# Optimization experiments

Measured on AMD Instinct MI355X. Metric: run time of the kernel, lower is better.

Reference implementation:

```python
import jax, jax.numpy as jnp
import numpy as np

# Static ragged block structure: (num_graphs_in_bucket, n) -> block tensor (B, n, n, C)
BLOCKS = [(128, 32), (64, 48), (32, 64), (16, 96)]
C = 64
DEPTH = 2
EPS = 1e-5
N_TOTAL = sum(b * n * n for b, n in BLOCKS)  # 557056


def _mlp(h, w, b):
    # stack of DEPTH Linear(C->C) + ReLU layers (1x1 convs in the torch module)
    for d in range(w.shape[0]):
        h = jax.nn.relu(jnp.einsum('...i,oi->...o', h, w[d]) + b[d])
    return h


def _bn(h, g, b, m, v):
    # eval-mode BatchNorm1d with running stats
    return g * (h - m) * jax.lax.rsqrt(v + EPS) + b


def setup_inputs() -> dict:
    key = jax.random.key(0)
    ks = jax.random.split(key, 8)
    s = 1.0 / np.sqrt(C)

    def lin(k):
        return jax.random.normal(k, (C, C), jnp.float32) * s

    return dict(
        x=jax.random.normal(ks[0], (N_TOTAL, C), jnp.float32),
        w_m1=jax.random.normal(ks[1], (DEPTH, C, C), jnp.float32) * s,
        b_m1=jnp.zeros((DEPTH, C), jnp.float32),
        w_m2=jax.random.normal(ks[2], (DEPTH, C, C), jnp.float32) * s,
        b_m2=jnp.zeros((DEPTH, C), jnp.float32),
        W_skip=lin(ks[3]), b_skip=jnp.zeros((C,), jnp.float32),
        W_u1=lin(ks[4]), b_u1=jnp.zeros((C,), jnp.float32),
        g1=jnp.ones((C,), jnp.float32), beta1=jnp.zeros((C,), jnp.float32),
        rm1=jnp.zeros((C,), jnp.float32), rv1=jnp.ones((C,), jnp.float32),
        W_u2=lin(ks[5]), b_u2=jnp.zeros((C,), jnp.float32),
        g2=jnp.ones((C,), jnp.float32), beta2=jnp.zeros((C,), jnp.float32),
        rm2=jnp.zeros((C,), jnp.float32), rv2=jnp.ones((C,), jnp.float32),
    )


def reference(x, w_m1, b_m1, w_m2, b_m2, W_skip, b_skip,
              W_u1, b_u1, g1, beta1, rm1, rv1,
              W_u2, b_u2, g2, beta2, rm2, rv2):
    # --- ragged split -> per-block PPGN-style matmul conv -> cat ---
    hs = []
    off = 0
    for (bnum, n) in BLOCKS:
        ln = bnum * n * n
        blk = x[off:off + ln].reshape(bnum, n, n, C)  # (B, n, n, C)
        m1 = _mlp(blk, w_m1, b_m1)
        m2 = _mlp(blk, w_m2, b_m2)
        # per-channel spatial matmul over the n x n block
        h = jnp.einsum('bijc,bjkc->bikc', m1, m2)
        hs.append(h.reshape(ln, C))
        off += ln
    hs2 = jnp.concatenate(hs, 0) + (x @ W_skip.T + b_skip)
    # --- update MLP: Linear-BN-ReLU-(Dropout eval=id)-Linear-BN-ReLU + residual ---
    u = jax.nn.relu(_bn(hs2 @ W_u1.T + b_u1, g1, beta1, rm1, rv1))
    u = jax.nn.relu(_bn(u @ W_u2.T + b_u2, g2, beta2, rm2, rv2))
    return u + hs2
```

## Files before the change

### kernel.cpp

```cpp
#include <hip/hip_runtime.h>
#include <hip/hip_bf16.h>

#define NT 557056
typedef __hip_bfloat16 bf16;
typedef __attribute__((ext_vector_type(8))) short short8;
typedef __attribute__((ext_vector_type(4))) short short4v;
typedef __attribute__((ext_vector_type(4))) float f32x4;


__device__ __forceinline__ short f2bs(float f){ bf16 h = __float2bfloat16(f); return *(short*)&h; }
__device__ __forceinline__ float s2f(short s){ bf16 h = *(bf16*)&s; return __bfloat162float(h); }

__device__ __forceinline__ short8 cvt8(float4 a, float4 b){
  short8 r;
  r[0]=f2bs(a.x); r[1]=f2bs(a.y); r[2]=f2bs(a.z); r[3]=f2bs(a.w);
  r[4]=f2bs(b.x); r[5]=f2bs(b.y); r[6]=f2bs(b.z); r[7]=f2bs(b.w);
  return r;
}
__device__ __forceinline__ short8 ldfrag(const float* __restrict__ p){
  return cvt8(*(const float4*)p, *(const float4*)(p + 4));
}
__device__ __forceinline__ short8 ldfrag_s(const float* __restrict__ p, float s){
  float4 a = *(const float4*)p, b = *(const float4*)(p + 4);
  a.x*=s; a.y*=s; a.z*=s; a.w*=s; b.x*=s; b.y*=s; b.z*=s; b.w*=s;
  return cvt8(a, b);
}
#define MFMA(a,b,c) __builtin_amdgcn_mfma_f32_16x16x32_bf16(a, b, c, 0, 0, 0)

#define LS 72

__global__ __launch_bounds__(256, 2) void k1_mlp(
    const float* __restrict__ x,
    const float* __restrict__ w_m1, const float* __restrict__ b_m1,
    const float* __restrict__ w_m2, const float* __restrict__ b_m2,
    bf16* __restrict__ m1t, bf16* __restrict__ m2t)
{
  __shared__ short yL[4][32][LS];
  const int tid = threadIdx.x;
  const int wv = tid >> 6, lane = tid & 63, r = lane & 15, g = lane >> 4;
  const int wid = blockIdx.x * 4 + wv;

  short8 wf[4][4][2];
  #pragma unroll
  for (int cb = 0; cb < 4; ++cb)
    #pragma unroll
    for (int s = 0; s < 2; ++s) {
      const int o = (cb*16 + r)*64 + s*32 + g*8;
      wf[0][cb][s] = ldfrag(w_m1 + o);
      wf[1][cb][s] = ldfrag(w_m1 + 4096 + o);
      wf[2][cb][s] = ldfrag(w_m2 + o);
      wf[3][cb][s] = ldfrag(w_m2 + 4096 + o);
    }
  f32x4 b0v[2][4];
  float b1v[2][4];
  #pragma unroll
  for (int m = 0; m < 2; ++m) {
    const float* bb = m ? b_m2 : b_m1;
    #pragma unroll
    for (int cb = 0; cb < 4; ++cb) {
      b0v[m][cb] = *(const f32x4*)(bb + cb*16 + 4*g);
      b1v[m][cb] = bb[64 + cb*16 + r];
    }
  }

  size_t pb = (size_t)wid * 128;

  float4 xr[8];
  #pragma unroll
  for (int h = 0; h < 2; ++h) {
    const float* xp = x + (pb + h*16 + r)*64 + g*8;
    xr[4*h+0] = *(const float4*)(xp);
    xr[4*h+1] = *(const float4*)(xp + 4);
    xr[4*h+2] = *(const float4*)(xp + 32);
    xr[4*h+3] = *(const float4*)(xp + 36);
  }

  for (int t = 0; t < 4; ++t, pb += 32) {
    short8 xf[2][2];
    xf[0][0] = cvt8(xr[0], xr[1]);  xf[0][1] = cvt8(xr[2], xr[3]);
    xf[1][0] = cvt8(xr[4], xr[5]);  xf[1][1] = cvt8(xr[6], xr[7]);
    if (t < 3) {
      #pragma unroll
      for (int h = 0; h < 2; ++h) {
        const float* xp = x + (pb + 32 + h*16 + r)*64 + g*8;
        xr[4*h+0] = *(const float4*)(xp);
        xr[4*h+1] = *(const float4*)(xp + 4);
        xr[4*h+2] = *(const float4*)(xp + 32);
        xr[4*h+3] = *(const float4*)(xp + 36);
      }
    }
    const size_t tbase = (pb >> 5) * 2048;
    #pragma unroll
    for (int m = 0; m < 2; ++m) {
      f32x4 acc[4][2];
      #pragma unroll
      for (int cb = 0; cb < 4; ++cb) { acc[cb][0] = b0v[m][cb]; acc[cb][1] = b0v[m][cb]; }
      #pragma unroll
      for (int cb = 0; cb < 4; ++cb)
        #pragma unroll
        for (int s = 0; s < 2; ++s) {
          acc[cb][0] = MFMA(wf[2*m][cb][s], xf[0][s], acc[cb][0]);
          acc[cb][1] = MFMA(wf[2*m][cb][s], xf[1][s], acc[cb][1]);
        }
      #pragma unroll
      for (int cb = 0; cb < 4; ++cb)
        #pragma unroll
        for (int th = 0; th < 2; ++th) {
          short4v v;
          #pragma unroll
          for (int q = 0; q < 4; ++q) v[q] = f2bs(fmaxf(acc[cb][th][q], 0.f));
          *(short4v*)&yL[wv][th*16 + r][cb*16 + 4*g] = v;
        }
      short8 af[2][2];
      #pragma unroll
      for (int th = 0; th < 2; ++th)
        #pragma unroll
        for (int s = 0; s < 2; ++s)
          af[th][s] = *(const short8*)&yL[wv][th*16 + r][s*32 + g*8];
      f32x4 acc2[4][2];
      #pragma unroll
      for (int cb = 0; cb < 4; ++cb) {
        const float bv = b1v[m][cb];
        acc2[cb][0] = (f32x4){bv,bv,bv,bv};
        acc2[cb][1] = (f32x4){bv,bv,bv,bv};
      }
      #pragma unroll
      for (int cb = 0; cb < 4; ++cb)
        #pragma unroll
        for (int s = 0; s < 2; ++s) {
          acc2[cb][0] = MFMA(af[0][s], wf[2*m+1][cb][s], acc2[cb][0]);
          acc2[cb][1] = MFMA(af[1][s], wf[2*m+1][cb][s], acc2[cb][1]);
        }
      bf16* op = m ? m2t : m1t;
      #pragma unroll
      for (int cb = 0; cb < 4; ++cb) {
        short8 v;
        #pragma unroll
        for (int th = 0; th < 2; ++th)
          #pragma unroll
          for (int q = 0; q < 4; ++q) v[th*4+q] = f2bs(fmaxf(acc2[cb][th][q], 0.f));
        *(short8*)(op + tbase + (cb*16 + r)*32 + g*8) = v;
      }
    }
  }
}

template<int N>
__global__ __launch_bounds__(256) void k2_spatial(
    const bf16* __restrict__ m1t, const bf16* __restrict__ m2t,
    bf16* __restrict__ ht, int off)
{
  constexpr int T = N / 16;
  constexpr int SA = N + 4;
  __shared__ __align__(16) float AT[N*SA];
  __shared__ __align__(16) float Bs[N*SA];
  const int b = blockIdx.x >> 6;
  const int c = blockIdx.x & 63;
  const size_t base_tile = ((size_t)off + (size_t)b * N * N) >> 5;
  const int tid = threadIdx.x;

  for (int idx8 = tid*8; idx8 < N*N; idx8 += 2048) {
    const size_t gaddr = (base_tile + (idx8 >> 5)) * 2048 + c*32 + (idx8 & 31);
    short8 a8 = *(const short8*)(m1t + gaddr);
    short8 b8 = *(const short8*)(m2t + gaddr);
    const int gsub = (idx8 & 31) >> 3;
    const int i0 = idx8 & ~31;
    #pragma unroll
    for (int th = 0; th < 2; ++th) {
      const int i = i0 + th*16 + 4*gsub;
      const int j = i / N, k0 = i - j*N;
      f32x4 bq;
      #pragma unroll
      for (int q = 0; q < 4; ++q) bq[q] = s2f(b8[th*4+q]);
      *(f32x4*)&Bs[j*SA + k0] = bq;
      #pragma unroll
      for (int q = 0; q < 4; ++q) AT[(k0+q)*SA + j] = s2f(a8[th*4+q]);
    }
  }
  __syncthreads();

  const int ti = tid >> 4, tk = tid & 15;
  float acc[T][T];
  #pragma unroll
  for (int ii = 0; ii < T; ++ii)
    #pragma unroll
    for (int kk = 0; kk < T; ++kk) acc[ii][kk] = 0.f;

  for (int j = 0; j < N; ++j) {
    const float* ar = &AT[j*SA + ti*T];
    const float* br = &Bs[j*SA + tk*T];
    float av[T], bv[T];
    if constexpr (T == 2) {
      float2 a2 = *(const float2*)ar; av[0]=a2.x; av[1]=a2.y;
      float2 b2 = *(const float2*)br; bv[0]=b2.x; bv[1]=b2.y;
    } else if constexpr (T == 3) {
      av[0]=ar[0]; av[1]=ar[1]; av[2]=ar[2];
      bv[0]=br[0]; bv[1]=br[1]; bv[2]=br[2];
    } else if constexpr (T == 4) {
      float4 a4 = *(const float4*)ar; av[0]=a4.x; av[1]=a4.y; av[2]=a4.z; av[3]=a4.w;
      float4 b4 = *(const float4*)br; bv[0]=b4.x; bv[1]=b4.y; bv[2]=b4.z; bv[3]=b4.w;
    } else {
      #pragma unroll
      for (int p = 0; p < 3; ++p) {
        float2 a2 = *(const float2*)(ar + 2*p); av[2*p]=a2.x; av[2*p+1]=a2.y;
        float2 b2 = *(const float2*)(br + 2*p); bv[2*p]=b2.x; bv[2*p+1]=b2.y;
      }
    }
    #pragma unroll
    for (int ii = 0; ii < T; ++ii)
      #pragma unroll
      for (int kk = 0; kk < T; ++kk)
        acc[ii][kk] = fmaf(av[ii], bv[kk], acc[ii][kk]);
  }

  __syncthreads();
  float* Cf = AT;
  #pragma unroll
  for (int ii = 0; ii < T; ++ii)
    #pragma unroll
    for (int kk = 0; kk < T; ++kk)
      Cf[(ti*T + ii)*N + tk*T + kk] = acc[ii][kk];
  __syncthreads();

  for (int idx8 = tid*8; idx8 < N*N; idx8 += 2048) {
    const int i0 = idx8 & ~31, gsub = (idx8 & 31) >> 3;
    f32x4 lo = *(const f32x4*)&Cf[i0 + 4*gsub];
    f32x4 hi = *(const f32x4*)&Cf[i0 + 16 + 4*gsub];
    short8 v;
    #pragma unroll
    for (int q = 0; q < 4; ++q) { v[q] = f2bs(lo[q]); v[4+q] = f2bs(hi[q]); }
    const size_t gaddr = (base_tile + (idx8 >> 5)) * 2048 + c*32 + (idx8 & 31);
    *(short8*)(ht + gaddr) = v;
  }
}

__global__ __launch_bounds__(256, 2) void k3_update(
    const float* __restrict__ x, const bf16* __restrict__ ht,
    const float* __restrict__ Wskip, const float* __restrict__ bskip,
    const float* __restrict__ Wu1, const float* __restrict__ bu1,
    const float* __restrict__ g1, const float* __restrict__ be1,
    const float* __restrict__ rm1, const float* __restrict__ rv1,
    const float* __restrict__ Wu2, const float* __restrict__ bu2,
    const float* __restrict__ g2, const float* __restrict__ be2,
    const float* __restrict__ rm2, const float* __restrict__ rv2,
    float* __restrict__ out)
{
  __shared__ short hs2L[4][32][LS];
  __shared__ short u1L[4][32][LS];
  const int tid = threadIdx.x;
  const int wv = tid >> 6, lane = tid & 63, r = lane & 15, g = lane >> 4;
  const int wid = blockIdx.x * 4 + wv;

  short8 wsk[4][2], w1f[4][2], w2f[4][2];
  float bskv[4];
  f32x4 b1c[4], b2c[4];
  #pragma unroll
  for (int cb = 0; cb < 4; ++cb) {
    const int row = cb*16 + r;
    const float s1 = g1[row] * rsqrtf(rv1[row] + 1e-5f);
    const float s2 = g2[row] * rsqrtf(rv2[row] + 1e-5f);
    #pragma unroll
    for (int s = 0; s < 2; ++s) {
      const int o = row*64 + s*32 + g*8;
      wsk[cb][s] = ldfrag(Wskip + o);
      w1f[cb][s] = ldfrag_s(Wu1 + o, s1);
      w2f[cb][s] = ldfrag_s(Wu2 + o, s2);
    }
    bskv[cb] = bskip[row];
    const int o4 = cb*16 + 4*g;
    f32x4 gg1 = *(const f32x4*)(g1 + o4),  vv1 = *(const f32x4*)(rv1 + o4);
    f32x4 mm1 = *(const f32x4*)(rm1 + o4), bb1 = *(const f32x4*)(be1 + o4);
    f32x4 u1b = *(const f32x4*)(bu1 + o4);
    f32x4 gg2 = *(const f32x4*)(g2 + o4),  vv2 = *(const f32x4*)(rv2 + o4);
    f32x4 mm2 = *(const f32x4*)(rm2 + o4), bb2 = *(const f32x4*)(be2 + o4);
    f32x4 u2b = *(const f32x4*)(bu2 + o4);
    #pragma unroll
    for (int q = 0; q < 4; ++q) {
      const float c1 = gg1[q] * rsqrtf(vv1[q] + 1e-5f);
      b1c[cb][q] = bb1[q] + (u1b[q] - mm1[q]) * c1;
      const float c2 = gg2[q] * rsqrtf(vv2[q] + 1e-5f);
      b2c[cb][q] = bb2[q] + (u2b[q] - mm2[q]) * c2;
    }
  }

  size_t pb = (size_t)wid * 128;

  float4 xr[8];
  #pragma unroll
  for (int h = 0; h < 2; ++h) {
    const float* xp = x + (pb + h*16 + r)*64 + g*8;
    xr[4*h+0] = *(const float4*)(xp);
    xr[4*h+1] = *(const float4*)(xp + 4);
    xr[4*h+2] = *(const float4*)(xp + 32);
    xr[4*h+3] = *(const float4*)(xp + 36);
  }

  for (int t = 0; t < 4; ++t, pb += 32) {
    short8 xf[2][2];
    xf[0][0] = cvt8(xr[0], xr[1]);  xf[0][1] = cvt8(xr[2], xr[3]);
    xf[1][0] = cvt8(xr[4], xr[5]);  xf[1][1] = cvt8(xr[6], xr[7]);
    if (t < 3) {
      #pragma unroll
      for (int h = 0; h < 2; ++h) {
        const float* xp = x + (pb + 32 + h*16 + r)*64 + g*8;
        xr[4*h+0] = *(const float4*)(xp);
        xr[4*h+1] = *(const float4*)(xp + 4);
        xr[4*h+2] = *(const float4*)(xp + 32);
        xr[4*h+3] = *(const float4*)(xp + 36);
      }
    }
    const size_t tbase = (pb >> 5) * 2048;
    short8 hv8[4];
    #pragma unroll
    for (int cb = 0; cb < 4; ++cb)
      hv8[cb] = *(const short8*)(ht + tbase + (cb*16 + r)*32 + g*8);

    f32x4 acc[4][2];
    #pragma unroll
    for (int cb = 0; cb < 4; ++cb) {
      acc[cb][0] = (f32x4){bskv[cb], bskv[cb], bskv[cb], bskv[cb]};
      acc[cb][1] = acc[cb][0];
    }
    #pragma unroll
    for (int cb = 0; cb < 4; ++cb)
      #pragma unroll
      for (int s = 0; s < 2; ++s) {
        acc[cb][0] = MFMA(xf[0][s], wsk[cb][s], acc[cb][0]);
        acc[cb][1] = MFMA(xf[1][s], wsk[cb][s], acc[cb][1]);
      }
    #pragma unroll
    for (int cb = 0; cb < 4; ++cb)
      #pragma unroll
      for (int th = 0; th < 2; ++th)
        #pragma unroll
        for (int q = 0; q < 4; ++q) acc[cb][th][q] += s2f(hv8[cb][th*4+q]);
    #pragma unroll
    for (int cb = 0; cb < 4; ++cb)
      #pragma unroll
      for (int th = 0; th < 2; ++th)
        #pragma unroll
        for (int q = 0; q < 4; ++q)
          hs2L[wv][th*16 + 4*g + q][cb*16 + r] = f2bs(acc[cb][th][q]);
    short8 hf[2][2];
    #pragma unroll
    for (int th = 0; th < 2; ++th)
      #pragma unroll
      for (int s = 0; s < 2; ++s)
        hf[th][s] = *(const short8*)&hs2L[wv][th*16 + r][s*32 + g*8];

    f32x4 a1[4][2];
    #pragma unroll
    for (int cb = 0; cb < 4; ++cb) { a1[cb][0] = b1c[cb]; a1[cb][1] = b1c[cb]; }
    #pragma unroll
    for (int cb = 0; cb < 4; ++cb)
      #pragma unroll
      for (int s = 0; s < 2; ++s) {
        a1[cb][0] = MFMA(w1f[cb][s], hf[0][s], a1[cb][0]);
        a1[cb][1] = MFMA(w1f[cb][s], hf[1][s], a1[cb][1]);
      }
    #pragma unroll
    for (int cb = 0; cb < 4; ++cb)
      #pragma unroll
      for (int th = 0; th < 2; ++th) {
        short4v v;
        #pragma unroll
        for (int q = 0; q < 4; ++q) v[q] = f2bs(fmaxf(a1[cb][th][q], 0.f));
        *(short4v*)&u1L[wv][th*16 + r][cb*16 + 4*g] = v;
      }
    short8 uf[2][2];
    #pragma unroll
    for (int th = 0; th < 2; ++th)
      #pragma unroll
      for (int s = 0; s < 2; ++s)
        uf[th][s] = *(const short8*)&u1L[wv][th*16 + r][s*32 + g*8];

    f32x4 a2[4][2];
    #pragma unroll
    for (int cb = 0; cb < 4; ++cb) { a2[cb][0] = b2c[cb]; a2[cb][1] = b2c[cb]; }
    #pragma unroll
    for (int cb = 0; cb < 4; ++cb)
      #pragma unroll
      for (int s = 0; s < 2; ++s) {
        a2[cb][0] = MFMA(w2f[cb][s], uf[0][s], a2[cb][0]);
        a2[cb][1] = MFMA(w2f[cb][s], uf[1][s], a2[cb][1]);
      }
    #pragma unroll
    for (int cb = 0; cb < 4; ++cb)
      #pragma unroll
      for (int th = 0; th < 2; ++th) {
        short4v hres = *(const short4v*)&hs2L[wv][th*16 + r][cb*16 + 4*g];
        f32x4 res;
        #pragma unroll
        for (int q = 0; q < 4; ++q)
          res[q] = fmaxf(a2[cb][th][q], 0.f) + s2f(hres[q]);
        *(f32x4*)(out + (pb + th*16 + r)*64 + cb*16 + 4*g) = res;
      }
  }
}

extern "C" void kernel_launch(void* const* d_in, const int* in_sizes, int n_in,
                              void* d_out, int out_size, void* d_ws, size_t ws_size,
                              hipStream_t stream) {
  const float* x     = (const float*)d_in[0];
  const float* w_m1  = (const float*)d_in[1];
  const float* b_m1  = (const float*)d_in[2];
  const float* w_m2  = (const float*)d_in[3];
  const float* b_m2  = (const float*)d_in[4];
  const float* Wskip = (const float*)d_in[5];
  const float* bskip = (const float*)d_in[6];
  const float* Wu1   = (const float*)d_in[7];
  const float* bu1   = (const float*)d_in[8];
  const float* g1    = (const float*)d_in[9];
  const float* be1   = (const float*)d_in[10];
  const float* rm1   = (const float*)d_in[11];
  const float* rv1   = (const float*)d_in[12];
  const float* Wu2   = (const float*)d_in[13];
  const float* bu2   = (const float*)d_in[14];
  const float* g2    = (const float*)d_in[15];
  const float* be2   = (const float*)d_in[16];
  const float* rm2   = (const float*)d_in[17];
  const float* rv2   = (const float*)d_in[18];
  float* out = (float*)d_out;

  bf16* m1t = (bf16*)d_ws;
  bf16* m2t = m1t + (size_t)64 * NT;
  bf16* ht  = m1t;

  k1_mlp<<<1088, 256, 0, stream>>>(x, w_m1, b_m1, w_m2, b_m2, m1t, m2t);

  k2_spatial<32><<<128*64, 256, 0, stream>>>(m1t, m2t, ht, 0);
  k2_spatial<48><<< 64*64, 256, 0, stream>>>(m1t, m2t, ht, 131072);
  k2_spatial<64><<< 32*64, 256, 0, stream>>>(m1t, m2t, ht, 278528);
  k2_spatial<96><<< 16*64, 256, 0, stream>>>(m1t, m2t, ht, 409600);

  k3_update<<<1088, 256, 0, stream>>>(x, ht, Wskip, bskip,
                                      Wu1, bu1, g1, be1, rm1, rv1,
                                      Wu2, bu2, g2, be2, rm2, rv2, out);
}
```

Baseline: 568.6 us.

## Replace scalar FP32 spatial matmul with bf16 MFMA kernel batching channels per block

The per-channel n×n spatial matmul kernel drops the FP32 FMA register-tiled loop and uses bf16 MFMA instructions reading fragments from LDS. Each block now processes several channels (CH), so global loads cover larger contiguous segments of the channel-interleaved layout. B is stored transposed and padded in LDS, and n=48 is zero-padded to the 32-wide K step. The added LDS staging and transposed scatter stores can cause bank conflicts, and inputs to the MFMA are in bf16 rather than being upcast to FP32.

New measurement: 544.6 us. 4.2% less time.

```diff
diff --git a/kernel.cpp b/kernel.cpp
--- a/kernel.cpp
+++ b/kernel.cpp
@@ -145,92 +145,92 @@
   }
 }
 
-template<int N>
-__global__ __launch_bounds__(256) void k2_spatial(
+template<int N, int CH, int NP, int CP>
+__global__ __launch_bounds__(256) void k2_mfma(
     const bf16* __restrict__ m1t, const bf16* __restrict__ m2t,
     bf16* __restrict__ ht, int off)
 {
-  constexpr int T = N / 16;
-  constexpr int SA = N + 4;
-  __shared__ __align__(16) float AT[N*SA];
-  __shared__ __align__(16) float Bs[N*SA];
-  const int b = blockIdx.x >> 6;
-  const int c = blockIdx.x & 63;
+  constexpr int TPB = N*N/32;
+  constexpr int NT16 = N/16;
+  constexpr int TPC = NT16*NT16;
+  constexpr int KS = (N + 31)/32;
+  constexpr int GRP = 64/CH;
+
+  __shared__ short Am[CH][N][NP];
+  __shared__ short Bt[CH][N][NP];
+  __shared__ short Cs[CH][N][CP];
+
+  const int tid = threadIdx.x;
+  const int grp = blockIdx.x % GRP;
+  const int b   = blockIdx.x / GRP;
+  const int c0  = grp * CH;
   const size_t base_tile = ((size_t)off + (size_t)b * N * N) >> 5;
-  const int tid = threadIdx.x;
-
-  for (int idx8 = tid*8; idx8 < N*N; idx8 += 2048) {
-    const size_t gaddr = (base_tile + (idx8 >> 5)) * 2048 + c*32 + (idx8 & 31);
-    short8 a8 = *(const short8*)(m1t + gaddr);
-    short8 b8 = *(const short8*)(m2t + gaddr);
-    const int gsub = (idx8 & 31) >> 3;
-    const int i0 = idx8 & ~31;
-    #pragma unroll
-    for (int th = 0; th < 2; ++th) {
-      const int i = i0 + th*16 + 4*gsub;
-      const int j = i / N, k0 = i - j*N;
-      f32x4 bq;
-      #pragma unroll
-      for (int q = 0; q < 4; ++q) bq[q] = s2f(b8[th*4+q]);
-      *(f32x4*)&Bs[j*SA + k0] = bq;
-      #pragma unroll
-      for (int q = 0; q < 4; ++q) AT[(k0+q)*SA + j] = s2f(a8[th*4+q]);
+
+  constexpr int UPT = CH * TPB * 4;
+  for (int u = tid; u < 2*UPT; u += 256) {
+    int uu = u;
+    const bf16* src = m1t;
+    bool isA = true;
+    if (uu >= UPT) { uu -= UPT; src = m2t; isA = false; }
+    const int a   = uu & 3;
+    const int cc  = (uu >> 2) % CH;
+    const int tau = (uu >> 2) / CH;
+    short8 v = *(const short8*)(src + (base_tile + tau)*2048 + (size_t)(c0+cc)*32 + a*8);
+    const int p0 = tau*32 + 4*a;
+    #pragma unroll
+    for (int h = 0; h < 2; ++h) {
+      const int p = p0 + h*16;
+      const int row = p / N, col = p % N;
+      if (isA) {
+        short4v w; w[0]=v[h*4+0]; w[1]=v[h*4+1]; w[2]=v[h*4+2]; w[3]=v[h*4+3];
+        *(short4v*)&Am[cc][row][col] = w;
+      } else {
+        #pragma unroll
+        for (int q = 0; q < 4; ++q) Bt[cc][col+q][row] = v[h*4+q];
+      }
+    }
+  }
+  if constexpr (N == 48) {
+    for (int u = tid; u < CH*N*4*2; u += 256) {
+      int uu = u; bool isA = uu < CH*N*4; if (!isA) uu -= CH*N*4;
+      const int seg = uu & 3, row = (uu>>2) % N, cc = (uu>>2) / N;
+      short4v z = {0,0,0,0};
+      if (isA) *(short4v*)&Am[cc][row][48 + seg*4] = z;
+      else     *(short4v*)&Bt[cc][row][48 + seg*4] = z;
     }
   }
   __syncthreads();
 
-  const int ti = tid >> 4, tk = tid & 15;
-  float acc[T][T];
-  #pragma unroll
-  for (int ii = 0; ii < T; ++ii)
-    #pragma unroll
-    for (int kk = 0; kk < T; ++kk) acc[ii][kk] = 0.f;
-
-  for (int j = 0; j < N; ++j) {
-    const float* ar = &AT[j*SA + ti*T];
-    const float* br = &Bs[j*SA + tk*T];
-    float av[T], bv[T];
-    if constexpr (T == 2) {
-      float2 a2 = *(const float2*)ar; av[0]=a2.x; av[1]=a2.y;
-      float2 b2 = *(const float2*)br; bv[0]=b2.x; bv[1]=b2.y;
-    } else if constexpr (T == 3) {
-      av[0]=ar[0]; av[1]=ar[1]; av[2]=ar[2];
-      bv[0]=br[0]; bv[1]=br[1]; bv[2]=br[2];
-    } else if constexpr (T == 4) {
-      float4 a4 = *(const float4*)ar; av[0]=a4.x; av[1]=a4.y; av[2]=a4.z; av[3]=a4.w;
-      float4 b4 = *(const float4*)br; bv[0]=b4.x; bv[1]=b4.y; bv[2]=b4.z; bv[3]=b4.w;
-    } else {
-      #pragma unroll
-      for (int p = 0; p < 3; ++p) {
-        float2 a2 = *(const float2*)(ar + 2*p); av[2*p]=a2.x; av[2*p+1]=a2.y;
-        float2 b2 = *(const float2*)(br + 2*p); bv[2*p]=b2.x; bv[2*p+1]=b2.y;
-      }
-    }
-    #pragma unroll
-    for (int ii = 0; ii < T; ++ii)
-      #pragma unroll
-      for (int kk = 0; kk < T; ++kk)
-        acc[ii][kk] = fmaf(av[ii], bv[kk], acc[ii][kk]);
-  }
-
+  const int wv = tid >> 6, lane = tid & 63, r = lane & 15, g = lane >> 4;
+  for (int idx = wv; idx < CH*TPC; idx += 4) {
+    const int cc = idx / TPC, t = idx % TPC;
+    const int i0 = (t / NT16) * 16, k0 = (t % NT16) * 16;
+    f32x4 acc = {0.f, 0.f, 0.f, 0.f};
+    #pragma unroll
+    for (int ks = 0; ks < KS; ++ks) {
+      short8 afr = *(const short8*)&Am[cc][i0 + r][ks*32 + g*8];
+      short8 bfr = *(const short8*)&Bt[cc][k0 + r][ks*32 + g*8];
+      acc = MFMA(afr, bfr, acc);
+    }
+    #pragma unroll
+    for (int q = 0; q < 4; ++q) Cs[cc][i0 + 4*g + q][k0 + r] = f2bs(acc[q]);
+  }
   __syncthreads();
-  float* Cf = AT;
-  #pragma unroll
-  for (int ii = 0; ii < T; ++ii)
-    #pragma unroll
-    for (int kk = 0; kk < T; ++kk)
-      Cf[(ti*T + ii)*N + tk*T + kk] = acc[ii][kk];
-  __syncthreads();
-
-  for (int idx8 = tid*8; idx8 < N*N; idx8 += 2048) {
-    const int i0 = idx8 & ~31, gsub = (idx8 & 31) >> 3;
-    f32x4 lo = *(const f32x4*)&Cf[i0 + 4*gsub];
-    f32x4 hi = *(const f32x4*)&Cf[i0 + 16 + 4*gsub];
+
+  for (int u = tid; u < UPT; u += 256) {
+    const int a   = u & 3;
+    const int cc  = (u >> 2) % CH;
+    const int tau = (u >> 2) / CH;
+    const int p0  = tau*32 + 4*a;
     short8 v;
     #pragma unroll
-    for (int q = 0; q < 4; ++q) { v[q] = f2bs(lo[q]); v[4+q] = f2bs(hi[q]); }
-    const size_t gaddr = (base_tile + (idx8 >> 5)) * 2048 + c*32 + (idx8 & 31);
-    *(short8*)(ht + gaddr) = v;
+    for (int h = 0; h < 2; ++h) {
+      const int p = p0 + h*16;
+      const int i = p / N, k = p % N;
+      short4v w = *(const short4v*)&Cs[cc][i][k];
+      v[h*4+0]=w[0]; v[h*4+1]=w[1]; v[h*4+2]=w[2]; v[h*4+3]=w[3];
+    }
+    *(short8*)(ht + (base_tile + tau)*2048 + (size_t)(c0+cc)*32 + a*8) = v;
   }
 }
 
@@ -428,10 +428,10 @@
 
   k1_mlp<<<1088, 256, 0, stream>>>(x, w_m1, b_m1, w_m2, b_m2, m1t, m2t);
 
-  k2_spatial<32><<<128*64, 256, 0, stream>>>(m1t, m2t, ht, 0);
-  k2_spatial<48><<< 64*64, 256, 0, stream>>>(m1t, m2t, ht, 131072);
-  k2_spatial<64><<< 32*64, 256, 0, stream>>>(m1t, m2t, ht, 278528);
-  k2_spatial<96><<< 16*64, 256, 0, stream>>>(m1t, m2t, ht, 409600);
+  k2_mfma<32, 8, 40,  40><<<128 *  8, 256, 0, stream>>>(m1t, m2t, ht, 0);
+  k2_mfma<48, 4, 72,  56><<< 64 * 16, 256, 0, stream>>>(m1t, m2t, ht, 131072);
+  k2_mfma<64, 2, 72,  72><<< 32 * 32, 256, 0, stream>>>(m1t, m2t, ht, 278528);
+  k2_mfma<96, 1, 104, 104><<< 16 * 64, 256, 0, stream>>>(m1t, m2t, ht, 409600);
 
   k3_update<<<1088, 256, 0, stream>>>(x, ht, Wskip, bskip,
                                       Wu1, bu1, g1, be1, rm1, rv1,
```
